# Kernel optimization log

Measured on AMD Instinct MI355X. Metric: run time of the kernel, lower is better.

Reference implementation:

```python
import jax, jax.numpy as jnp
import numpy as np

N_NODES = 200000
N_EDGES = 200000
N_GRAPHS = 128
IN_FEATS, HID_FEATS, OUT_FEATS = 256, 128, 128


def gcn_conv(x, W, b, src, dst, n_nodes):
    """PyG-style GCNConv: add self-loops, symmetric deg^-1/2 normalization."""
    h = x @ W  # [N, out]
    # degree with self-loops: deg[i] = 1 + (# edges with target i)
    deg = 1.0 + jax.ops.segment_sum(jnp.ones(src.shape[0], x.dtype), dst,
                                    num_segments=n_nodes)
    dinv = jax.lax.rsqrt(deg)
    norm = dinv[src] * dinv[dst]  # per-edge coeff
    agg = jax.ops.segment_sum(h[src] * norm[:, None], dst, num_segments=n_nodes)
    agg = agg + h * (1.0 / deg)[:, None]  # self-loop contribution
    return agg + b


def setup_inputs() -> dict:
    key = jax.random.key(0)
    k = jax.random.split(key, 8)
    x = jax.random.normal(k[0], (N_NODES, IN_FEATS), jnp.float32)
    edge_index = jax.random.randint(k[1], (2, N_EDGES), 0, N_NODES)
    batch = jnp.sort(jax.random.randint(k[2], (N_NODES,), 0, N_GRAPHS))
    root_index = jax.random.randint(k[3], (N_GRAPHS,), 0, N_NODES)
    # GCNConv params (xavier-ish scale)
    W1 = jax.random.normal(k[4], (IN_FEATS, HID_FEATS), jnp.float32) * (2.0 / (IN_FEATS + HID_FEATS)) ** 0.5
    b1 = jnp.zeros((HID_FEATS,), jnp.float32)
    W2 = jax.random.normal(k[5], (HID_FEATS + IN_FEATS, OUT_FEATS), jnp.float32) * (2.0 / (HID_FEATS + IN_FEATS + OUT_FEATS)) ** 0.5
    b2 = jnp.zeros((OUT_FEATS,), jnp.float32)
    return {"x": x, "edge_index": edge_index, "batch": batch,
            "root_index": root_index, "W1": W1, "b1": b1, "W2": W2, "b2": b2}


def reference(x, edge_index, batch, root_index, W1, b1, W2, b2):
    src, dst = edge_index[0], edge_index[1]
    x1 = x  # raw input features
    h = gcn_conv(x, W1, b1, src, dst, N_NODES)  # conv1 -> [N, hid]
    x2 = h
    # root broadcast: root_extend[i] = x1[root_index[batch[i]]]
    root_extend = x1[root_index[batch]]  # [N, in]
    h = jnp.concatenate([h, root_extend], axis=1)  # [N, hid+in]
    h = jax.nn.relu(h)
    # F.dropout(training=self.training): eval mode -> identity
    h = gcn_conv(h, W2, b2, src, dst, N_NODES)  # conv2 -> [N, out]
    h = jax.nn.relu(h)
    root_extend2 = x2[root_index[batch]]  # [N, hid]
    h = jnp.concatenate([h, root_extend2], axis=1)  # [N, out+hid]
    # scatter_mean over graphs
    sums = jax.ops.segment_sum(h, batch, num_segments=N_GRAPHS)
    counts = jax.ops.segment_sum(jnp.ones((N_NODES,), h.dtype), batch,
                                 num_segments=N_GRAPHS)
    return sums / jnp.maximum(counts, 1.0)[:, None]  # [B, out+hid]
```

## Files before the change

### kernel.cpp

```cpp
#include <hip/hip_runtime.h>
#include <stddef.h>

constexpr int N_NODES = 200000;
constexpr int N_EDGES = 200000;
constexpr int N_GRAPHS = 128;
constexpr int IN_F = 256;
constexpr int HID_F = 128;
constexpr int OUT_F = 128;
constexpr int OUT_W = OUT_F + HID_F;
constexpr int SCAN_NB = (N_NODES + 1023) / 1024;

typedef __attribute__((ext_vector_type(8))) short short8;
typedef __attribute__((ext_vector_type(4))) float float4v;

__device__ __forceinline__ short f2bf(float f) {
    union { float f; unsigned u; } v; v.f = f;
    unsigned r = v.u + 0x7fffu + ((v.u >> 16) & 1u);
    return (short)(r >> 16);
}
__device__ __forceinline__ float bf2f(unsigned short s) {
    union { unsigned u; float f; } v; v.u = ((unsigned)s) << 16;
    return v.f;
}


__global__ void edge_prep_kernel(const int* __restrict__ dst, int* __restrict__ cntin, int E) {
    int e = blockIdx.x * blockDim.x + threadIdx.x;
    if (e < E) atomicAdd(&cntin[dst[e]], 1);
}


__global__ __launch_bounds__(1024) void scan_reduce_kernel(const int* __restrict__ cnt,
                                                           int* __restrict__ partial, int n) {
    __shared__ int sm[1024];
    int t = threadIdx.x;
    int i = blockIdx.x * 1024 + t;
    sm[t] = (i < n) ? cnt[i] : 0;
    __syncthreads();
    for (int ofs = 512; ofs > 0; ofs >>= 1) {
        if (t < ofs) sm[t] += sm[t + ofs];
        __syncthreads();
    }
    if (t == 0) partial[blockIdx.x] = sm[0];
}

__global__ void scan_base_kernel(int* __restrict__ partial, int nb) {
    __shared__ int sm[256];
    int t = threadIdx.x;
    sm[t] = (t < nb) ? partial[t] : 0;
    __syncthreads();
    for (int ofs = 1; ofs < 256; ofs <<= 1) {
        int v = (t >= ofs) ? sm[t - ofs] : 0;
        __syncthreads();
        sm[t] += v;
        __syncthreads();
    }
    if (t < nb) partial[t] = (t == 0) ? 0 : sm[t - 1];
}

__global__ __launch_bounds__(1024) void scan_final_kernel(const int* __restrict__ cnt,
                                                          const int* __restrict__ partial,
                                                          int* __restrict__ rp,
                                                          int* __restrict__ cur,
                                                          float* __restrict__ dinv, int n) {
    __shared__ int sm[1024];
    int t = threadIdx.x;
    int i = blockIdx.x * 1024 + t;
    int v = (i < n) ? cnt[i] : 0;
    sm[t] = v;
    __syncthreads();
    for (int ofs = 1; ofs < 1024; ofs <<= 1) {
        int u = (t >= ofs) ? sm[t - ofs] : 0;
        __syncthreads();
        sm[t] += u;
        __syncthreads();
    }
    int base = partial[blockIdx.x];
    if (i < n) {
        int ex = base + sm[t] - v;
        rp[i] = ex;
        cur[i] = ex;
        dinv[i] = rsqrtf(1.0f + (float)v);
        if (i == n - 1) rp[n] = ex + v;
    }
}

__global__ void bucket_kernel(const int* __restrict__ src, const int* __restrict__ dst,
                              int* __restrict__ cur, int* __restrict__ adj, int E) {
    int e = blockIdx.x * blockDim.x + threadIdx.x;
    if (e < E) {
        int pos = atomicAdd(&cur[dst[e]], 1);
        adj[pos] = src[e];
    }
}

__global__ void bounds_kernel(const int* __restrict__ batch, int* __restrict__ start,
                              int* __restrict__ cnt, int n, int G) {
    __shared__ int s_start[N_GRAPHS + 1];
    int g = threadIdx.x;
    if (g < G) {
        int lo = 0, hi = n;
        while (lo < hi) {
            int mid = (lo + hi) >> 1;
            if (batch[mid] < g) lo = mid + 1; else hi = mid;
        }
        s_start[g] = lo;
        if (g == 0) s_start[G] = n;
    }
    __syncthreads();
    if (g < G) {
        start[g] = s_start[g];
        cnt[g] = s_start[g + 1] - s_start[g];
    }
}

__global__ void transpose_w_kernel(const float* __restrict__ W1, const float* __restrict__ W2,
                                   short* __restrict__ Bt1, short* __restrict__ Bt2) {
    int k = blockIdx.x;
    int n = threadIdx.x;
    if (k < IN_F) {
        Bt1[(size_t)n * IN_F + k] = f2bf(W1[(size_t)k * 128 + n]);
    } else {
        int kk = k - IN_F;
        Bt2[(size_t)n * HID_F + kk] = f2bf(W2[(size_t)kk * 128 + n]);
    }
}

__global__ void rootlin_kernel(const float* __restrict__ x, const int* __restrict__ root_index,
                               const float* __restrict__ W2, float* __restrict__ rootlin)
{
    int g = blockIdx.x;
    int f = threadIdx.x;
    int r = root_index[g];
    const float* xr = x + (size_t)r * IN_F;
    float acc = 0.f;
    for (int k = 0; k < IN_F; ++k) {
        float xv = fmaxf(xr[k], 0.f);
        acc += xv * W2[(size_t)(HID_F + k) * OUT_F + f];
    }
    rootlin[(size_t)g * OUT_F + f] = acc;
}

template<int KTOT, bool GATHER, bool ADDROOT>
__global__ __launch_bounds__(256) void mfma_gemm_kernel(
    const void* __restrict__ Ap, const short* __restrict__ Bt,
    unsigned short* __restrict__ outp,
    const float* __restrict__ dinv, const float* __restrict__ bvec,
    const float* __restrict__ rootlin, const int* __restrict__ batch,
    const int* __restrict__ rp, const int* __restrict__ adj)
{
    __shared__ __align__(16) short As[64][136];
    __shared__ __align__(16) short Bs[128][136];

    const int tid = threadIdx.x;
    const int wave = tid >> 6;
    const int lane = tid & 63;
    const int quad = lane >> 4;
    const int l16  = lane & 15;
    const int row0 = blockIdx.x * 64;

    float4v acc[8];
    #pragma unroll
    for (int c = 0; c < 8; ++c) acc[c] = (float4v){0.f, 0.f, 0.f, 0.f};

    const int arow = tid >> 2;
    const int ac8 = (tid & 3) * 8;
    const int bn = tid >> 1;
    const int bk = (tid & 1) * 64;

    for (int kb = 0; kb < KTOT / 128; ++kb) {
        {
            const short* bp = Bt + (size_t)bn * KTOT + kb * 128 + bk;
            #pragma unroll
            for (int j = 0; j < 8; ++j)
                *(short8*)&Bs[bn][bk + 8 * j] = *(const short8*)(bp + 8 * j);
        }
        if (GATHER) {
            const unsigned short* A = (const unsigned short*)Ap;
            const int row = row0 + arow;
            float sum[4][8];
            const unsigned short* hp = A + (size_t)row * 128 + ac8;
            #pragma unroll
            for (int jj = 0; jj < 4; ++jj) {
                short8 h = *(const short8*)(hp + 32 * jj);
                #pragma unroll
                for (int q = 0; q < 8; ++q) sum[jj][q] = bf2f((unsigned short)h[q]);
            }
            int e0 = rp[row], e1 = rp[row + 1];
            for (int e = e0; e < e1; ++e) {
                const unsigned short* qp = A + (size_t)adj[e] * 128 + ac8;
                #pragma unroll
                for (int jj = 0; jj < 4; ++jj) {
                    short8 h = *(const short8*)(qp + 32 * jj);
                    #pragma unroll
                    for (int q = 0; q < 8; ++q) sum[jj][q] += bf2f((unsigned short)h[q]);
                }
            }
            float asc = dinv[row];
            #pragma unroll
            for (int jj = 0; jj < 4; ++jj) {
                const float* bv = bvec + ac8 + 32 * jj;
                short8 s;
                #pragma unroll
                for (int q = 0; q < 8; ++q)
                    s[q] = f2bf(fmaxf(asc * sum[jj][q] + bv[q], 0.f));
                *(short8*)&As[arow][ac8 + 32 * jj] = s;
            }
        } else {
            const float* A = (const float*)Ap;
            const float* ap = A + (size_t)(row0 + arow) * KTOT + kb * 128 + ac8;
            #pragma unroll
            for (int jj = 0; jj < 4; ++jj) {
                float4 f0 = *(const float4*)(ap + 32 * jj);
                float4 f1 = *(const float4*)(ap + 32 * jj + 4);
                short8 s;
                s[0] = f2bf(f0.x); s[1] = f2bf(f0.y); s[2] = f2bf(f0.z); s[3] = f2bf(f0.w);
                s[4] = f2bf(f1.x); s[5] = f2bf(f1.y); s[6] = f2bf(f1.z); s[7] = f2bf(f1.w);
                *(short8*)&As[arow][ac8 + 32 * jj] = s;
            }
        }
        __syncthreads();
        #pragma unroll
        for (int ks = 0; ks < 4; ++ks) {
            short8 af = *(const short8*)&As[wave * 16 + l16][ks * 32 + quad * 8];
            #pragma unroll
            for (int c = 0; c < 8; ++c) {
                short8 bf = *(const short8*)&Bs[c * 16 + l16][ks * 32 + quad * 8];
                acc[c] = __builtin_amdgcn_mfma_f32_16x16x32_bf16(af, bf, acc[c], 0, 0, 0);
            }
        }
        __syncthreads();
    }

    #pragma unroll
    for (int r = 0; r < 4; ++r) {
        int row = row0 + wave * 16 + quad * 4 + r;
        float di = dinv[row];
        const float* rl = nullptr;
        if (ADDROOT) rl = rootlin + (size_t)batch[row] * 128;
        #pragma unroll
        for (int c = 0; c < 8; ++c) {
            int col = c * 16 + l16;
            float v = acc[c][r];
            if (ADDROOT) v += rl[col];
            outp[(size_t)row * 128 + col] = (unsigned short)f2bf(v * di);
        }
    }
}

__global__ void mean_kernel(const unsigned short* __restrict__ hs2,
                            const unsigned short* __restrict__ hs1,
                            const float* __restrict__ dinv, const float* __restrict__ b1v,
                            const float* __restrict__ b2v, const int* __restrict__ root_index,
                            const int* __restrict__ cnt, const int* __restrict__ start,
                            const int* __restrict__ rp, const int* __restrict__ adj,
                            float* __restrict__ out, int chunks)
{
    int g = blockIdx.x;
    int c = blockIdx.y;
    int f = threadIdx.x;
    int s = start[g], n = cnt[g];
    int per = (n + chunks - 1) / chunks;
    int lo = s + c * per;
    int hi = min(s + n, lo + per);
    float bb = b2v[f];
    float accv = 0.f;
    for (int i = lo; i < hi; ++i) {
        float v = bf2f(hs2[(size_t)i * 128 + f]);
        int e0 = rp[i], e1 = rp[i + 1];
        for (int e = e0; e < e1; ++e)
            v += bf2f(hs2[(size_t)adj[e] * 128 + f]);
        accv += fmaxf(dinv[i] * v + bb, 0.f);
    }
    if (hi > lo)
        atomicAdd(&out[(size_t)g * OUT_W + f], accv / (float)max(n, 1));
    if (c == 0) {
        int r = root_index[g];
        float v = 0.f;
        if (n > 0) {
            v = bf2f(hs1[(size_t)r * 128 + f]);
            int e0 = rp[r], e1 = rp[r + 1];
            for (int e = e0; e < e1; ++e)
                v += bf2f(hs1[(size_t)adj[e] * 128 + f]);
            v = dinv[r] * v + b1v[f];
        }
        out[(size_t)g * OUT_W + HID_F + f] = v;
    }
}


static inline size_t align_up(size_t x, size_t a) { return (x + a - 1) / a * a; }

extern "C" void kernel_launch(void* const* d_in, const int* in_sizes, int n_in,
                              void* d_out, int out_size, void* d_ws, size_t ws_size,
                              hipStream_t stream) {
    const float* x = (const float*)d_in[0];
    const int* ei = (const int*)d_in[1];
    const int* batch = (const int*)d_in[2];
    const int* root = (const int*)d_in[3];
    const float* W1 = (const float*)d_in[4];
    const float* b1 = (const float*)d_in[5];
    const float* W2 = (const float*)d_in[6];
    const float* b2 = (const float*)d_in[7];
    float* out = (float*)d_out;

    const int* src = ei;
    const int* dst = ei + N_EDGES;

    char* ws = (char*)d_ws;
    size_t off = 0;
    const size_t NB16 = (size_t)N_NODES * 128 * sizeof(unsigned short);

    float* dinv = (float*)(ws + off);    off = align_up(off + (size_t)N_NODES * sizeof(float), 256);
    int* cnt = (int*)(ws + off);         off = align_up(off + N_GRAPHS * sizeof(int), 256);
    int* startv = (int*)(ws + off);      off = align_up(off + N_GRAPHS * sizeof(int), 256);
    float* rootlin = (float*)(ws + off); off = align_up(off + (size_t)N_GRAPHS * OUT_F * sizeof(float), 256);
    short* Bt1 = (short*)(ws + off);     off = align_up(off + (size_t)128 * IN_F * sizeof(short), 256);
    short* Bt2 = (short*)(ws + off);     off = align_up(off + (size_t)128 * HID_F * sizeof(short), 256);
    int* rowptr = (int*)(ws + off);      off = align_up(off + (size_t)(N_NODES + 1) * sizeof(int), 256);
    int* cursor = (int*)(ws + off);      off = align_up(off + (size_t)N_NODES * sizeof(int), 256);
    int* partial = (int*)(ws + off);     off = align_up(off + (size_t)SCAN_NB * sizeof(int), 256);
    int* adj = (int*)(ws + off);         off = align_up(off + (size_t)N_EDGES * sizeof(int), 256);
    unsigned short* hs1 = (unsigned short*)(ws + off); off = align_up(off + NB16, 256);
    unsigned short* hs2 = (unsigned short*)(ws + off); off = align_up(off + NB16, 256);
    (void)ws_size; (void)n_in; (void)in_sizes; (void)out_size;

    hipMemsetAsync(cursor, 0, (size_t)N_NODES * sizeof(int), stream);
    edge_prep_kernel<<<(N_EDGES + 255) / 256, 256, 0, stream>>>(dst, cursor, N_EDGES);
    scan_reduce_kernel<<<SCAN_NB, 1024, 0, stream>>>(cursor, partial, N_NODES);
    scan_base_kernel<<<1, 256, 0, stream>>>(partial, SCAN_NB);
    scan_final_kernel<<<SCAN_NB, 1024, 0, stream>>>(cursor, partial, rowptr, cursor, dinv, N_NODES);
    bucket_kernel<<<(N_EDGES + 255) / 256, 256, 0, stream>>>(src, dst, cursor, adj, N_EDGES);
    bounds_kernel<<<1, N_GRAPHS, 0, stream>>>(batch, startv, cnt, N_NODES, N_GRAPHS);

    transpose_w_kernel<<<IN_F + HID_F, 128, 0, stream>>>(W1, W2, Bt1, Bt2);
    rootlin_kernel<<<N_GRAPHS, OUT_F, 0, stream>>>(x, root, W2, rootlin);

    mfma_gemm_kernel<IN_F, false, false><<<N_NODES / 64, 256, 0, stream>>>(
        x, Bt1, hs1, dinv, nullptr, nullptr, nullptr, nullptr, nullptr);

    mfma_gemm_kernel<HID_F, true, true><<<N_NODES / 64, 256, 0, stream>>>(
        hs1, Bt2, hs2, dinv, b1, rootlin, batch, rowptr, adj);

    hipMemsetAsync(out, 0, (size_t)N_GRAPHS * OUT_W * sizeof(float), stream);
    dim3 mg(N_GRAPHS, 32);
    mean_kernel<<<mg, 128, 0, stream>>>(hs2, hs1, dinv, b1, b2, root, cnt, startv,
                                        rowptr, adj, out, 32);
}
```

Baseline: 457.2 us.

## Fuse preprocessing kernels into one persistent kernel with grid barriers

```diff
diff --git a/kernel.cpp b/kernel.cpp
--- a/kernel.cpp
+++ b/kernel.cpp
@@ -8,7 +8,12 @@
 constexpr int HID_F = 128;
 constexpr int OUT_F = 128;
 constexpr int OUT_W = OUT_F + HID_F;
-constexpr int SCAN_NB = (N_NODES + 1023) / 1024;
+
+constexpr int PRE_NB = 1024;
+constexpr int PRE_T = PRE_NB * 256;
+static_assert(N_NODES <= PRE_T, "single-shot node phases");
+static_assert(N_EDGES <= PRE_T, "single-shot edge phases");
+static_assert(N_EDGES <= PRE_T - N_GRAPHS * OUT_F, "rootlin threads disjoint from edge threads");
 
 typedef __attribute__((ext_vector_type(8))) short short8;
 typedef __attribute__((ext_vector_type(4))) float float4v;
@@ -23,122 +28,123 @@
     return v.f;
 }
 
-
-__global__ void edge_prep_kernel(const int* __restrict__ dst, int* __restrict__ cntin, int E) {
-    int e = blockIdx.x * blockDim.x + threadIdx.x;
-    if (e < E) atomicAdd(&cntin[dst[e]], 1);
-}
-
-
-__global__ __launch_bounds__(1024) void scan_reduce_kernel(const int* __restrict__ cnt,
-                                                           int* __restrict__ partial, int n) {
-    __shared__ int sm[1024];
-    int t = threadIdx.x;
-    int i = blockIdx.x * 1024 + t;
-    sm[t] = (i < n) ? cnt[i] : 0;
+__device__ __forceinline__ void grid_bar(int* bar, int idx, int nb) {
     __syncthreads();
-    for (int ofs = 512; ofs > 0; ofs >>= 1) {
-        if (t < ofs) sm[t] += sm[t + ofs];
-        __syncthreads();
-    }
-    if (t == 0) partial[blockIdx.x] = sm[0];
-}
-
-__global__ void scan_base_kernel(int* __restrict__ partial, int nb) {
+    if (threadIdx.x == 0) {
+        __threadfence();
+        __hip_atomic_fetch_add(&bar[idx], 1, __ATOMIC_RELEASE, __HIP_MEMORY_SCOPE_AGENT);
+        while (__hip_atomic_load(&bar[idx], __ATOMIC_ACQUIRE, __HIP_MEMORY_SCOPE_AGENT) < nb)
+            __builtin_amdgcn_s_sleep(2);
+        __threadfence();
+    }
+    __syncthreads();
+}
+
+__global__ __launch_bounds__(256, 4) void pre_fused_kernel(
+    const int* __restrict__ src, const int* __restrict__ dst,
+    const int* __restrict__ batch, const int* __restrict__ root_index,
+    const float* __restrict__ x, const float* __restrict__ W1,
+    const float* __restrict__ W2,
+    int* __restrict__ cntcur,
+    int* __restrict__ rp,
+    int* __restrict__ adj,
+    int* __restrict__ partial,
+    float* __restrict__ dinv,
+    int* __restrict__ startv, int* __restrict__ cntg,
+    short* __restrict__ Bt1, short* __restrict__ Bt2,
+    float* __restrict__ rootlin, float* __restrict__ out,
+    int* __restrict__ bar)
+{
     __shared__ int sm[256];
-    int t = threadIdx.x;
-    sm[t] = (t < nb) ? partial[t] : 0;
+    const int t = threadIdx.x;
+    const int gid = blockIdx.x * 256 + t;
+
+    if (gid < N_NODES) cntcur[gid] = 0;
+    if (gid < 128 * IN_F) {
+        int n = gid >> 8, k = gid & 255;
+        Bt1[n * IN_F + k] = f2bf(W1[(size_t)k * 128 + n]);
+    }
+    if (gid < 128 * HID_F) {
+        int n = gid >> 7, k = gid & 127;
+        Bt2[n * HID_F + k] = f2bf(W2[(size_t)k * 128 + n]);
+    }
+    if (gid < N_GRAPHS * OUT_W) out[gid] = 0.f;
+    if (gid < N_GRAPHS) {
+        int g = gid;
+        int lo = 0, hi = N_NODES;
+        while (lo < hi) { int mid = (lo + hi) >> 1; if (batch[mid] < g) lo = mid + 1; else hi = mid; }
+        int lo2 = N_NODES;
+        if (g != N_GRAPHS - 1) {
+            int a = lo, b = N_NODES;
+            while (a < b) { int mid = (a + b) >> 1; if (batch[mid] < g + 1) a = mid + 1; else b = mid; }
+            lo2 = a;
+        }
+        startv[g] = lo;
+        cntg[g] = lo2 - lo;
+    }
+    grid_bar(bar, 0, PRE_NB);
+
+    if (gid < N_EDGES) {
+        atomicAdd(&cntcur[dst[gid]], 1);
+    } else if (gid >= PRE_T - N_GRAPHS * OUT_F) {
+        int idx = gid - (PRE_T - N_GRAPHS * OUT_F);
+        int g = idx >> 7, f = idx & 127;
+        int r = root_index[g];
+        const float* xr = x + (size_t)r * IN_F;
+        float acc = 0.f;
+        for (int k = 0; k < IN_F; ++k)
+            acc += fmaxf(xr[k], 0.f) * W2[(size_t)(HID_F + k) * OUT_F + f];
+        rootlin[(size_t)g * OUT_F + f] = acc;
+    }
+    grid_bar(bar, 1, PRE_NB);
+
+    int v = (gid < N_NODES) ? cntcur[gid] : 0;
+    sm[t] = v;
     __syncthreads();
     for (int ofs = 1; ofs < 256; ofs <<= 1) {
-        int v = (t >= ofs) ? sm[t - ofs] : 0;
-        __syncthreads();
-        sm[t] += v;
-        __syncthreads();
-    }
-    if (t < nb) partial[t] = (t == 0) ? 0 : sm[t - 1];
-}
-
-__global__ __launch_bounds__(1024) void scan_final_kernel(const int* __restrict__ cnt,
-                                                          const int* __restrict__ partial,
-                                                          int* __restrict__ rp,
-                                                          int* __restrict__ cur,
-                                                          float* __restrict__ dinv, int n) {
-    __shared__ int sm[1024];
-    int t = threadIdx.x;
-    int i = blockIdx.x * 1024 + t;
-    int v = (i < n) ? cnt[i] : 0;
-    sm[t] = v;
-    __syncthreads();
-    for (int ofs = 1; ofs < 1024; ofs <<= 1) {
         int u = (t >= ofs) ? sm[t - ofs] : 0;
         __syncthreads();
         sm[t] += u;
         __syncthreads();
     }
+    int lex = sm[t] - v;
+    if (t == 255) partial[blockIdx.x] = sm[255];
+    grid_bar(bar, 2, PRE_NB);
+
+    if (blockIdx.x == 0) {
+        int p0 = partial[t * 4 + 0], p1 = partial[t * 4 + 1];
+        int p2 = partial[t * 4 + 2], p3 = partial[t * 4 + 3];
+        int ts = p0 + p1 + p2 + p3;
+        sm[t] = ts;
+        __syncthreads();
+        for (int ofs = 1; ofs < 256; ofs <<= 1) {
+            int u = (t >= ofs) ? sm[t - ofs] : 0;
+            __syncthreads();
+            sm[t] += u;
+            __syncthreads();
+        }
+        int ex = sm[t] - ts;
+        partial[t * 4 + 0] = ex;
+        partial[t * 4 + 1] = ex + p0;
+        partial[t * 4 + 2] = ex + p0 + p1;
+        partial[t * 4 + 3] = ex + p0 + p1 + p2;
+    }
+    grid_bar(bar, 3, PRE_NB);
+
     int base = partial[blockIdx.x];
-    if (i < n) {
-        int ex = base + sm[t] - v;
-        rp[i] = ex;
-        cur[i] = ex;
-        dinv[i] = rsqrtf(1.0f + (float)v);
-        if (i == n - 1) rp[n] = ex + v;
-    }
-}
-
-__global__ void bucket_kernel(const int* __restrict__ src, const int* __restrict__ dst,
-                              int* __restrict__ cur, int* __restrict__ adj, int E) {
-    int e = blockIdx.x * blockDim.x + threadIdx.x;
-    if (e < E) {
-        int pos = atomicAdd(&cur[dst[e]], 1);
-        adj[pos] = src[e];
-    }
-}
-
-__global__ void bounds_kernel(const int* __restrict__ batch, int* __restrict__ start,
-                              int* __restrict__ cnt, int n, int G) {
-    __shared__ int s_start[N_GRAPHS + 1];
-    int g = threadIdx.x;
-    if (g < G) {
-        int lo = 0, hi = n;
-        while (lo < hi) {
-            int mid = (lo + hi) >> 1;
-            if (batch[mid] < g) lo = mid + 1; else hi = mid;
-        }
-        s_start[g] = lo;
-        if (g == 0) s_start[G] = n;
-    }
-    __syncthreads();
-    if (g < G) {
-        start[g] = s_start[g];
-        cnt[g] = s_start[g + 1] - s_start[g];
-    }
-}
-
-__global__ void transpose_w_kernel(const float* __restrict__ W1, const float* __restrict__ W2,
-                                   short* __restrict__ Bt1, short* __restrict__ Bt2) {
-    int k = blockIdx.x;
-    int n = threadIdx.x;
-    if (k < IN_F) {
-        Bt1[(size_t)n * IN_F + k] = f2bf(W1[(size_t)k * 128 + n]);
-    } else {
-        int kk = k - IN_F;
-        Bt2[(size_t)n * HID_F + kk] = f2bf(W2[(size_t)kk * 128 + n]);
-    }
-}
-
-__global__ void rootlin_kernel(const float* __restrict__ x, const int* __restrict__ root_index,
-                               const float* __restrict__ W2, float* __restrict__ rootlin)
-{
-    int g = blockIdx.x;
-    int f = threadIdx.x;
-    int r = root_index[g];
-    const float* xr = x + (size_t)r * IN_F;
-    float acc = 0.f;
-    for (int k = 0; k < IN_F; ++k) {
-        float xv = fmaxf(xr[k], 0.f);
-        acc += xv * W2[(size_t)(HID_F + k) * OUT_F + f];
-    }
-    rootlin[(size_t)g * OUT_F + f] = acc;
+    if (gid < N_NODES) {
+        int ex = base + lex;
+        rp[gid] = ex;
+        cntcur[gid] = ex;
+        dinv[gid] = rsqrtf(1.0f + (float)v);
+        if (gid == N_NODES - 1) rp[N_NODES] = ex + v;
+    }
+    grid_bar(bar, 4, PRE_NB);
+
+    if (gid < N_EDGES) {
+        int pos = atomicAdd(&cntcur[dst[gid]], 1);
+        adj[pos] = src[gid];
+    }
 }
 
 template<int KTOT, bool GATHER, bool ADDROOT>
@@ -312,29 +318,26 @@
     const size_t NB16 = (size_t)N_NODES * 128 * sizeof(unsigned short);
 
     float* dinv = (float*)(ws + off);    off = align_up(off + (size_t)N_NODES * sizeof(float), 256);
-    int* cnt = (int*)(ws + off);         off = align_up(off + N_GRAPHS * sizeof(int), 256);
+    int* cntg = (int*)(ws + off);        off = align_up(off + N_GRAPHS * sizeof(int), 256);
     int* startv = (int*)(ws + off);      off = align_up(off + N_GRAPHS * sizeof(int), 256);
     float* rootlin = (float*)(ws + off); off = align_up(off + (size_t)N_GRAPHS * OUT_F * sizeof(float), 256);
     short* Bt1 = (short*)(ws + off);     off = align_up(off + (size_t)128 * IN_F * sizeof(short), 256);
     short* Bt2 = (short*)(ws + off);     off = align_up(off + (size_t)128 * HID_F * sizeof(short), 256);
     int* rowptr = (int*)(ws + off);      off = align_up(off + (size_t)(N_NODES + 1) * sizeof(int), 256);
-    int* cursor = (int*)(ws + off);      off = align_up(off + (size_t)N_NODES * sizeof(int), 256);
-    int* partial = (int*)(ws + off);     off = align_up(off + (size_t)SCAN_NB * sizeof(int), 256);
+    int* cntcur = (int*)(ws + off);      off = align_up(off + (size_t)N_NODES * sizeof(int), 256);
+    int* partial = (int*)(ws + off);     off = align_up(off + (size_t)PRE_NB * sizeof(int), 256);
+    int* bar = (int*)(ws + off);         off = align_up(off + 8 * sizeof(int), 256);
     int* adj = (int*)(ws + off);         off = align_up(off + (size_t)N_EDGES * sizeof(int), 256);
     unsigned short* hs1 = (unsigned short*)(ws + off); off = align_up(off + NB16, 256);
     unsigned short* hs2 = (unsigned short*)(ws + off); off = align_up(off + NB16, 256);
     (void)ws_size; (void)n_in; (void)in_sizes; (void)out_size;
 
-    hipMemsetAsync(cursor, 0, (size_t)N_NODES * sizeof(int), stream);
-    edge_prep_kernel<<<(N_EDGES + 255) / 256, 256, 0, stream>>>(dst, cursor, N_EDGES);
-    scan_reduce_kernel<<<SCAN_NB, 1024, 0, stream>>>(cursor, partial, N_NODES);
-    scan_base_kernel<<<1, 256, 0, stream>>>(partial, SCAN_NB);
-    scan_final_kernel<<<SCAN_NB, 1024, 0, stream>>>(cursor, partial, rowptr, cursor, dinv, N_NODES);
-    bucket_kernel<<<(N_EDGES + 255) / 256, 256, 0, stream>>>(src, dst, cursor, adj, N_EDGES);
-    bounds_kernel<<<1, N_GRAPHS, 0, stream>>>(batch, startv, cnt, N_NODES, N_GRAPHS);
-
-    transpose_w_kernel<<<IN_F + HID_F, 128, 0, stream>>>(W1, W2, Bt1, Bt2);
-    rootlin_kernel<<<N_GRAPHS, OUT_F, 0, stream>>>(x, root, W2, rootlin);
+    hipMemsetAsync(bar, 0, 8 * sizeof(int), stream);
+
+    pre_fused_kernel<<<PRE_NB, 256, 0, stream>>>(
+        src, dst, batch, root, x, W1, W2,
+        cntcur, rowptr, adj, partial, dinv, startv, cntg,
+        Bt1, Bt2, rootlin, out, bar);
 
     mfma_gemm_kernel<IN_F, false, false><<<N_NODES / 64, 256, 0, stream>>>(
         x, Bt1, hs1, dinv, nullptr, nullptr, nullptr, nullptr, nullptr);
@@ -342,8 +345,7 @@
     mfma_gemm_kernel<HID_F, true, true><<<N_NODES / 64, 256, 0, stream>>>(
         hs1, Bt2, hs2, dinv, b1, rootlin, batch, rowptr, adj);
 
-    hipMemsetAsync(out, 0, (size_t)N_GRAPHS * OUT_W * sizeof(float), stream);
     dim3 mg(N_GRAPHS, 32);
-    mean_kernel<<<mg, 128, 0, stream>>>(hs2, hs1, dinv, b1, b2, root, cnt, startv,
+    mean_kernel<<<mg, 128, 0, stream>>>(hs2, hs1, dinv, b1, b2, root, cntg, startv,
                                         rowptr, adj, out, 32);
 }
```

Result: slower. 1.313 ms (+187.2%).

## Split conv2 neighbor gather into separate kernel and widen rootlin/mean parallelism

Applied to the files above, without the earlier changes.

```diff
diff --git a/kernel.cpp b/kernel.cpp
--- a/kernel.cpp
+++ b/kernel.cpp
@@ -28,7 +28,6 @@
     int e = blockIdx.x * blockDim.x + threadIdx.x;
     if (e < E) atomicAdd(&cntin[dst[e]], 1);
 }
-
 
 __global__ __launch_bounds__(1024) void scan_reduce_kernel(const int* __restrict__ cnt,
                                                            int* __restrict__ partial, int n) {
@@ -130,24 +129,67 @@
                                const float* __restrict__ W2, float* __restrict__ rootlin)
 {
     int g = blockIdx.x;
+    int s = blockIdx.y;
     int f = threadIdx.x;
     int r = root_index[g];
     const float* xr = x + (size_t)r * IN_F;
     float acc = 0.f;
-    for (int k = 0; k < IN_F; ++k) {
+    int k0 = s * (IN_F / 4);
+    for (int k = k0; k < k0 + IN_F / 4; ++k) {
         float xv = fmaxf(xr[k], 0.f);
         acc += xv * W2[(size_t)(HID_F + k) * OUT_F + f];
     }
-    rootlin[(size_t)g * OUT_F + f] = acc;
-}
-
-template<int KTOT, bool GATHER, bool ADDROOT>
+    atomicAdd(&rootlin[(size_t)g * OUT_F + f], acc);
+}
+
+__global__ __launch_bounds__(256) void agg2_kernel(
+    const unsigned short* __restrict__ hs1, const float* __restrict__ dinv,
+    const float* __restrict__ b1v, const int* __restrict__ rp,
+    const int* __restrict__ adj, unsigned short* __restrict__ hsag)
+{
+    int gid = blockIdx.x * 256 + threadIdx.x;
+    int r = gid >> 3;
+    int c0 = (gid & 7) * 16;
+    const unsigned short* hp = hs1 + (size_t)r * 128 + c0;
+    float sum[16];
+    {
+        short8 h0 = *(const short8*)hp;
+        short8 h1 = *(const short8*)(hp + 8);
+        #pragma unroll
+        for (int q = 0; q < 8; ++q) {
+            sum[q] = bf2f((unsigned short)h0[q]);
+            sum[8 + q] = bf2f((unsigned short)h1[q]);
+        }
+    }
+    int e0 = rp[r], e1 = rp[r + 1];
+    for (int e = e0; e < e1; ++e) {
+        const unsigned short* qp = hs1 + (size_t)adj[e] * 128 + c0;
+        short8 h0 = *(const short8*)qp;
+        short8 h1 = *(const short8*)(qp + 8);
+        #pragma unroll
+        for (int q = 0; q < 8; ++q) {
+            sum[q] += bf2f((unsigned short)h0[q]);
+            sum[8 + q] += bf2f((unsigned short)h1[q]);
+        }
+    }
+    float di = dinv[r];
+    short8 s0, s1;
+    #pragma unroll
+    for (int q = 0; q < 8; ++q) {
+        s0[q] = f2bf(fmaxf(di * sum[q] + b1v[c0 + q], 0.f));
+        s1[q] = f2bf(fmaxf(di * sum[8 + q] + b1v[c0 + 8 + q], 0.f));
+    }
+    unsigned short* op = hsag + (size_t)r * 128 + c0;
+    *(short8*)op = s0;
+    *(short8*)(op + 8) = s1;
+}
+
+template<int KTOT, bool ABF16, bool ADDROOT>
 __global__ __launch_bounds__(256) void mfma_gemm_kernel(
     const void* __restrict__ Ap, const short* __restrict__ Bt,
     unsigned short* __restrict__ outp,
-    const float* __restrict__ dinv, const float* __restrict__ bvec,
-    const float* __restrict__ rootlin, const int* __restrict__ batch,
-    const int* __restrict__ rp, const int* __restrict__ adj)
+    const float* __restrict__ dinv,
+    const float* __restrict__ rootlin, const int* __restrict__ batch)
 {
     __shared__ __align__(16) short As[64][136];
     __shared__ __align__(16) short Bs[128][136];
@@ -175,37 +217,12 @@
             for (int j = 0; j < 8; ++j)
                 *(short8*)&Bs[bn][bk + 8 * j] = *(const short8*)(bp + 8 * j);
         }
-        if (GATHER) {
+        if (ABF16) {
             const unsigned short* A = (const unsigned short*)Ap;
-            const int row = row0 + arow;
-            float sum[4][8];
-            const unsigned short* hp = A + (size_t)row * 128 + ac8;
+            const unsigned short* ap = A + (size_t)(row0 + arow) * KTOT + kb * 128 + ac8;
             #pragma unroll
-            for (int jj = 0; jj < 4; ++jj) {
-                short8 h = *(const short8*)(hp + 32 * jj);
-                #pragma unroll
-                for (int q = 0; q < 8; ++q) sum[jj][q] = bf2f((unsigned short)h[q]);
-            }
-            int e0 = rp[row], e1 = rp[row + 1];
-            for (int e = e0; e < e1; ++e) {
-                const unsigned short* qp = A + (size_t)adj[e] * 128 + ac8;
-                #pragma unroll
-                for (int jj = 0; jj < 4; ++jj) {
-                    short8 h = *(const short8*)(qp + 32 * jj);
-                    #pragma unroll
-                    for (int q = 0; q < 8; ++q) sum[jj][q] += bf2f((unsigned short)h[q]);
-                }
-            }
-            float asc = dinv[row];
-            #pragma unroll
-            for (int jj = 0; jj < 4; ++jj) {
-                const float* bv = bvec + ac8 + 32 * jj;
-                short8 s;
-                #pragma unroll
-                for (int q = 0; q < 8; ++q)
-                    s[q] = f2bf(fmaxf(asc * sum[jj][q] + bv[q], 0.f));
-                *(short8*)&As[arow][ac8 + 32 * jj] = s;
-            }
+            for (int jj = 0; jj < 4; ++jj)
+                *(short8*)&As[arow][ac8 + 32 * jj] = *(const short8*)(ap + 32 * jj);
         } else {
             const float* A = (const float*)Ap;
             const float* ap = A + (size_t)(row0 + arow) * KTOT + kb * 128 + ac8;
@@ -312,7 +329,7 @@
     const size_t NB16 = (size_t)N_NODES * 128 * sizeof(unsigned short);
 
     float* dinv = (float*)(ws + off);    off = align_up(off + (size_t)N_NODES * sizeof(float), 256);
-    int* cnt = (int*)(ws + off);         off = align_up(off + N_GRAPHS * sizeof(int), 256);
+    int* cntg = (int*)(ws + off);        off = align_up(off + N_GRAPHS * sizeof(int), 256);
     int* startv = (int*)(ws + off);      off = align_up(off + N_GRAPHS * sizeof(int), 256);
     float* rootlin = (float*)(ws + off); off = align_up(off + (size_t)N_GRAPHS * OUT_F * sizeof(float), 256);
     short* Bt1 = (short*)(ws + off);     off = align_up(off + (size_t)128 * IN_F * sizeof(short), 256);
@@ -321,8 +338,9 @@
     int* cursor = (int*)(ws + off);      off = align_up(off + (size_t)N_NODES * sizeof(int), 256);
     int* partial = (int*)(ws + off);     off = align_up(off + (size_t)SCAN_NB * sizeof(int), 256);
     int* adj = (int*)(ws + off);         off = align_up(off + (size_t)N_EDGES * sizeof(int), 256);
-    unsigned short* hs1 = (unsigned short*)(ws + off); off = align_up(off + NB16, 256);
-    unsigned short* hs2 = (unsigned short*)(ws + off); off = align_up(off + NB16, 256);
+    unsigned short* hs1 = (unsigned short*)(ws + off);  off = align_up(off + NB16, 256);
+    unsigned short* hs2 = (unsigned short*)(ws + off);  off = align_up(off + NB16, 256);
+    unsigned short* hsag = (unsigned short*)(ws + off); off = align_up(off + NB16, 256);
     (void)ws_size; (void)n_in; (void)in_sizes; (void)out_size;
 
     hipMemsetAsync(cursor, 0, (size_t)N_NODES * sizeof(int), stream);
@@ -331,19 +349,24 @@
     scan_base_kernel<<<1, 256, 0, stream>>>(partial, SCAN_NB);
     scan_final_kernel<<<SCAN_NB, 1024, 0, stream>>>(cursor, partial, rowptr, cursor, dinv, N_NODES);
     bucket_kernel<<<(N_EDGES + 255) / 256, 256, 0, stream>>>(src, dst, cursor, adj, N_EDGES);
-    bounds_kernel<<<1, N_GRAPHS, 0, stream>>>(batch, startv, cnt, N_NODES, N_GRAPHS);
+    bounds_kernel<<<1, N_GRAPHS, 0, stream>>>(batch, startv, cntg, N_NODES, N_GRAPHS);
 
     transpose_w_kernel<<<IN_F + HID_F, 128, 0, stream>>>(W1, W2, Bt1, Bt2);
-    rootlin_kernel<<<N_GRAPHS, OUT_F, 0, stream>>>(x, root, W2, rootlin);
+    hipMemsetAsync(rootlin, 0, (size_t)N_GRAPHS * OUT_F * sizeof(float), stream);
+    dim3 rg(N_GRAPHS, 4);
+    rootlin_kernel<<<rg, OUT_F, 0, stream>>>(x, root, W2, rootlin);
 
     mfma_gemm_kernel<IN_F, false, false><<<N_NODES / 64, 256, 0, stream>>>(
-        x, Bt1, hs1, dinv, nullptr, nullptr, nullptr, nullptr, nullptr);
+        x, Bt1, hs1, dinv, nullptr, nullptr);
+
+    agg2_kernel<<<(N_NODES * 8) / 256, 256, 0, stream>>>(hs1, dinv, b1, rowptr, adj, hsag);
 
     mfma_gemm_kernel<HID_F, true, true><<<N_NODES / 64, 256, 0, stream>>>(
-        hs1, Bt2, hs2, dinv, b1, rootlin, batch, rowptr, adj);
+        hsag, Bt2, hs2, dinv, rootlin, batch);
 
     hipMemsetAsync(out, 0, (size_t)N_GRAPHS * OUT_W * sizeof(float), stream);
-    dim3 mg(N_GRAPHS, 32);
-    mean_kernel<<<mg, 128, 0, stream>>>(hs2, hs1, dinv, b1, b2, root, cnt, startv,
-                                        rowptr, adj, out, 32);
-}
+    constexpr int CHUNKS = 128;
+    dim3 mg(N_GRAPHS, CHUNKS);
+    mean_kernel<<<mg, 128, 0, stream>>>(hs2, hs1, dinv, b1, b2, root, cntg, startv,
+                                        rowptr, adj, out, CHUNKS);
+}
```

New measurement: 459.8 us. No clear change (+0.6%).
